# Kernel optimization log

Hardware: AMD Instinct MI355X
Metric: run time of the kernel (lower is better)

The kernel has to match this reference:

```python
import jax, jax.numpy as jnp
import numpy as np

B, D, H, W = 32, 64, 64, 64
K = 512  # num_embeddings


def _l2norm(x, axis):
    return x / jnp.linalg.norm(x, axis=axis, keepdims=True)


def setup_inputs() -> dict:
    key = jax.random.key(0)
    k1, k2 = jax.random.split(key)
    # continuous latents, normalized on the unit sphere along channel dim D
    z_e = _l2norm(jax.random.normal(k1, (B, D, H, W), jnp.float32), axis=1)
    # codebook: uniform(-1,1) then row-normalized (as in torch __init__)
    emb_weight = _l2norm(
        jax.random.uniform(k2, (K, D), jnp.float32, -1.0, 1.0), axis=1)
    kappa = jnp.float32(1.0)
    return {"z_e": z_e, "emb_weight": emb_weight, "kappa": kappa}


def reference(z_e, emb_weight, kappa):
    b, d, h, w = z_e.shape
    # [B,D,H,W] -> [N,D] tokens
    flat_z = z_e.transpose(0, 2, 3, 1).reshape(-1, d)
    emb_w = _l2norm(emb_weight, axis=1)            # [K,D]
    sims = flat_z @ emb_w.T                        # [N,K]
    logits = kappa * sims
    # categorical sampling == torch.multinomial over softmax(logits)
    indices = jax.random.categorical(jax.random.key(42), logits, axis=-1)  # [N]
    z_q = emb_w[indices].reshape(b, h, w, d).transpose(0, 3, 1, 2)  # [B,D,H,W]
    chosen_sims = jnp.take_along_axis(sims, indices[:, None], axis=1)[:, 0]
    reg = jnp.mean(kappa * (1.0 - chosen_sims))
    return z_q, reg, indices.reshape(b, h, w)
```

## Files before the change

kernel.cpp:

```cpp
#include <hip/hip_runtime.h>
#include <stdint.h>

#define K_CODES 512
#define N_TOK   131072
#define ZQ_ELEMS 8388608
#define ZS_STRIDE 68
#define ECSTRIDE 65

__device__ __forceinline__ uint32_t rotl32(uint32_t x, int d) {
#if __has_builtin(__builtin_amdgcn_alignbit)
  return __builtin_amdgcn_alignbit(x, x, 32 - d);
#else
  return (x << d) | (x >> (32 - d));
#endif
}

template <int CTRL, int RMASK>
__device__ __forceinline__ float dpp_add_f32(float x) {
  int d = __builtin_amdgcn_update_dpp(0, __builtin_bit_cast(int, x),
                                      CTRL, RMASK, 0xf, true);
  return x + __builtin_bit_cast(float, d);
}
template <int CTRL, int RMASK>
__device__ __forceinline__ uint32_t dpp_max_u32(uint32_t x) {
  uint32_t d = (uint32_t)__builtin_amdgcn_update_dpp(0, (int)x,
                                                     CTRL, RMASK, 0xf, true);
  return x > d ? x : d;
}
__device__ __forceinline__ float wave_sum(float x) {
  x = dpp_add_f32<0x111, 0xf>(x);
  x = dpp_add_f32<0x112, 0xf>(x);
  x = dpp_add_f32<0x114, 0xf>(x);
  x = dpp_add_f32<0x118, 0xf>(x);
  x = dpp_add_f32<0x142, 0xa>(x);
  x = dpp_add_f32<0x143, 0xc>(x);
  return __builtin_bit_cast(float,
      __builtin_amdgcn_readlane(__builtin_bit_cast(int, x), 63));
}
__device__ __forceinline__ uint32_t wave_max(uint32_t x) {
  x = dpp_max_u32<0x111, 0xf>(x);
  x = dpp_max_u32<0x112, 0xf>(x);
  x = dpp_max_u32<0x114, 0xf>(x);
  x = dpp_max_u32<0x118, 0xf>(x);
  x = dpp_max_u32<0x142, 0xa>(x);
  x = dpp_max_u32<0x143, 0xc>(x);
  return (uint32_t)__builtin_amdgcn_readlane((int)x, 63);
}

__device__ __forceinline__ uint32_t tf_bits_xor(uint32_t lo) {
  const uint32_t ks0 = 0u, ks1 = 42u, ks2 = 0x1BD11BDAu ^ 0u ^ 42u;
  uint32_t x0 = 0u;
  uint32_t x1 = lo + ks1;
#define TFR(r) { x0 += x1; x1 = rotl32(x1, (r)); x1 ^= x0; }
  TFR(13) TFR(15) TFR(26) TFR(6)
  x0 += ks1; x1 += ks2 + 1u;
  TFR(17) TFR(29) TFR(16) TFR(24)
  x0 += ks2; x1 += ks0 + 2u;
  TFR(13) TFR(15) TFR(26) TFR(6)
  x0 += ks0; x1 += ks1 + 3u;
  TFR(17) TFR(29) TFR(16) TFR(24)
  x0 += ks1; x1 += ks2 + 4u;
  TFR(13) TFR(15) TFR(26) TFR(6)
  x0 += ks2; x1 += ks0 + 5u;
#undef TFR
  return x0 ^ x1;
}

__device__ __forceinline__ float g_of_u23(uint32_t u23) {
  float u0 = (float)u23 * 0x1p-23f;
  float u  = fmaxf(u0 + 1.17549435e-38f, 1.17549435e-38f);
  float nl = -logf(u);
  return -logf(nl);
}

__device__ __forceinline__ float g_fast_u23(uint32_t u23) {
  uint32_t m = 8388608u - u23;
  float nl;
  if (m <= 131072u) {
    float x = (float)m * 0x1p-23f;
    nl = x * fmaf(x, fmaf(x, fmaf(x, 0.25f, 0.33333334f), 0.5f), 1.0f);
  } else {
    float u = (float)u23 * 0x1p-23f;
    nl = -__logf(u);
  }
  return -__logf(nl);
}

__device__ __forceinline__ uint32_t thr_fast(float gthr) {
  float u_t = __expf(-__expf(-gthr));
  int B = (int)floorf(u_t * 8388608.0f) - 64;
  if (B < 0) B = 0;
  return ((uint32_t)B) << 9;
}

__global__ void k_norm(const float* __restrict__ w, float* __restrict__ embn) {
  int k = blockIdx.x;
  int d = threadIdx.x;
  float v = w[(k << 6) + d];
  float s = v * v;
#pragma unroll
  for (int off = 1; off < 64; off <<= 1) s += __shfl_xor(s, off);
  embn[(k << 6) + d] = v / sqrtf(s);
}

__global__ __launch_bounds__(1024, 8) void k_top(
    const float* __restrict__ z_e, const float* __restrict__ embn,
    const float* __restrict__ kappa_p, int* __restrict__ idx_ws,
    float* __restrict__ partials, float* __restrict__ out_idx) {
  __shared__ float zs[16 * ZS_STRIDE];
  __shared__ float redbuf[16];

  const float kappa = kappa_p[0];
  const int tid = threadIdx.x;
  const int wv = tid >> 6;
  const int lane = tid & 63;
  const int t0 = blockIdx.x * 16;
  const int t = t0 + wv;
  const int b = t0 >> 12, h = (t0 >> 6) & 63, w0 = t0 & 63;
  const float* zb = z_e + (b << 18) + (h << 6) + w0;

  {
    int wloc = tid & 15;
    int d = tid >> 4;
    zs[wloc * ZS_STRIDE + d] = zb[(d << 12) + wloc];
  }
  __syncthreads();
  const float zv = zs[wv * ZS_STRIDE + lane];

  const uint32_t base = ((uint32_t)t << 9) + (uint32_t)(lane << 3);
  uint32_t p[8];
  uint32_t rm = 0;
#pragma unroll
  for (int j = 0; j < 8; ++j) {
    uint32_t bits = tf_bits_xor(base + (uint32_t)j);
    uint32_t pk = (bits & 0xFFFFFE00u) | (uint32_t)((lane << 3) + j);
    p[j] = pk;
    rm = rm > pk ? rm : pk;
  }
  rm = wave_max(rm);

  float best, bsim, best2 = -INFINITY;
  int bk;
  {
    int k = (int)(rm & 511u);
    float e = embn[(k << 6) + lane];
    float pr = wave_sum(zv * e);
    best = fmaf(kappa, pr, g_fast_u23(rm >> 9));
    bsim = pr;
    bk = k;
  }
  uint32_t cut = thr_fast(best - 1.0001f * kappa - 0.001f);

#pragma unroll
  for (int j = 0; j < 8; ++j) {
    unsigned long long m = __ballot(p[j] >= cut);
    while (m) {
      int L = __ffsll(m) - 1;
      m &= m - 1;
      uint32_t pk = __shfl(p[j], L);
      if (pk == rm) continue;
      if (pk < cut) continue;
      int k = (int)(pk & 511u);
      float e = embn[(k << 6) + lane];
      float pr = wave_sum(zv * e);
      float v = fmaf(kappa, pr, g_fast_u23(pk >> 9));
      if (v > best) {
        best2 = best;
        best = v; bk = k; bsim = pr;
        cut = thr_fast(best - 1.0001f * kappa - 0.001f);
      } else if (v > best2) {
        best2 = v;
      }
    }
  }

  if (best - best2 < 2e-4f) {
    best = -INFINITY; bsim = 0.0f; bk = 0;
#pragma unroll
    for (int j = 0; j < 8; ++j) {
      unsigned long long m = __ballot(p[j] >= cut);
      while (m) {
        int L = __ffsll(m) - 1;
        m &= m - 1;
        uint32_t pk = __shfl(p[j], L);
        int k = (int)(pk & 511u);
        float e = embn[(k << 6) + lane];
        float pr = wave_sum(zv * e);
        float gg = g_of_u23(pk >> 9);
        float v = fmaf(kappa, pr, gg);
        if (v > best || (v == best && k < bk)) { best = v; bk = k; bsim = pr; }
      }
    }
  }

  if (lane == 0) {
    idx_ws[t] = bk;
    out_idx[t] = (float)bk;
    redbuf[wv] = kappa * (1.0f - bsim);
  }
  __syncthreads();
  if (tid == 0) {
    float s = 0.f;
#pragma unroll
    for (int i = 0; i < 16; ++i) s += redbuf[i];
    partials[blockIdx.x] = s;
  }
}

__global__ __launch_bounds__(256) void k_reg(const float* __restrict__ partials,
                                             float* __restrict__ out_reg) {
  int tid = threadIdx.x;
  float s = 0.f;
#pragma unroll
  for (int j = 0; j < 32; ++j) s += partials[(j << 8) + tid];
#pragma unroll
  for (int off = 32; off; off >>= 1) s += __shfl_down(s, off);
  __shared__ float l[4];
  int lane = tid & 63, wid = tid >> 6;
  if (lane == 0) l[wid] = s;
  __syncthreads();
  if (tid == 0) out_reg[0] = ((l[0] + l[1]) + (l[2] + l[3])) * (1.0f / 131072.0f);
}

__global__ __launch_bounds__(256) void k_gather(
    const float* __restrict__ embn, const int* __restrict__ idx_ws,
    float* __restrict__ out_zq) {
  __shared__ float erow[64 * ECSTRIDE];
  __shared__ int sidx[64];
  int blk = blockIdx.x;
  int b = blk >> 6, h = blk & 63;
  int tid = threadIdx.x;
  int lane = tid & 63, wid = tid >> 6;

  if (tid < 64) sidx[tid] = idx_ws[(b << 12) + (h << 6) + tid];
  __syncthreads();
  for (int r = wid; r < 64; r += 4)
    erow[r * ECSTRIDE + lane] = embn[(sidx[r] << 6) + lane];
  __syncthreads();

  int w = tid & 63;
  int d0 = tid >> 6;
  float* outp = out_zq + (b << 18) + (h << 6) + w;
#pragma unroll
  for (int i = 0; i < 16; ++i) {
    int d = (i << 2) + d0;
    outp[d << 12] = erow[w * ECSTRIDE + d];
  }
}

extern "C" void kernel_launch(void* const* d_in, const int* in_sizes, int n_in,
                              void* d_out, int out_size, void* d_ws, size_t ws_size,
                              hipStream_t stream) {
  const float* z_e    = (const float*)d_in[0];
  const float* emb_w  = (const float*)d_in[1];
  const float* kappa  = (const float*)d_in[2];

  float* embn     = (float*)d_ws;
  int*   idx_ws   = (int*)((char*)d_ws + 131072);
  float* partials = (float*)((char*)d_ws + 131072 + 524288);

  float* out     = (float*)d_out;
  float* out_zq  = out;
  float* out_reg = out + ZQ_ELEMS;
  float* out_idx = out + ZQ_ELEMS + 1;

  k_norm  <<<K_CODES, 64, 0, stream>>>(emb_w, embn);
  k_top   <<<N_TOK / 16, 1024, 0, stream>>>(z_e, embn, kappa, idx_ws, partials, out_idx);
  k_reg   <<<1, 256, 0, stream>>>(partials, out_reg);
  k_gather<<<2048, 256, 0, stream>>>(embn, idx_ws, out_zq);
}
```

Measured before the change: 167.0 us.

## Score surviving candidates per lane instead of serial wave-wide dot products

Candidate scoring in the Gumbel-max sampler is reorganized. The old code processed candidates one at a time across the whole wave: a ballot, a shuffle, a 64-wide dot product and a DPP reduction for each. Now each lane scores its own surviving candidates, reading codebook rows from global memory and broadcasting z components with readlane. It keeps a per-lane top-2 and finishes with wave-wide fmax reductions. The cutoff is fixed from the seed and no longer tightened as better candidates appear, and the exact tie-break now compares only the top two instead of rescanning all candidates. This may prune less and adds per-lane uncoalesced 256-byte row loads.

```diff
diff --git a/kernel.cpp b/kernel.cpp
--- a/kernel.cpp
+++ b/kernel.cpp
@@ -20,6 +20,12 @@
   int d = __builtin_amdgcn_update_dpp(0, __builtin_bit_cast(int, x),
                                       CTRL, RMASK, 0xf, true);
   return x + __builtin_bit_cast(float, d);
+}
+template <int CTRL, int RMASK>
+__device__ __forceinline__ float dpp_max_f32(float x) {
+  int d = __builtin_amdgcn_update_dpp(0, __builtin_bit_cast(int, x),
+                                      CTRL, RMASK, 0xf, true);
+  return fmaxf(x, __builtin_bit_cast(float, d));
 }
 template <int CTRL, int RMASK>
 __device__ __forceinline__ uint32_t dpp_max_u32(uint32_t x) {
@@ -37,7 +43,17 @@
   return __builtin_bit_cast(float,
       __builtin_amdgcn_readlane(__builtin_bit_cast(int, x), 63));
 }
-__device__ __forceinline__ uint32_t wave_max(uint32_t x) {
+__device__ __forceinline__ float wave_fmax(float x) {
+  x = dpp_max_f32<0x111, 0xf>(x);
+  x = dpp_max_f32<0x112, 0xf>(x);
+  x = dpp_max_f32<0x114, 0xf>(x);
+  x = dpp_max_f32<0x118, 0xf>(x);
+  x = dpp_max_f32<0x142, 0xa>(x);
+  x = dpp_max_f32<0x143, 0xc>(x);
+  return __builtin_bit_cast(float,
+      __builtin_amdgcn_readlane(__builtin_bit_cast(int, x), 63));
+}
+__device__ __forceinline__ uint32_t wave_max_u32(uint32_t x) {
   x = dpp_max_u32<0x111, 0xf>(x);
   x = dpp_max_u32<0x112, 0xf>(x);
   x = dpp_max_u32<0x114, 0xf>(x);
@@ -45,6 +61,13 @@
   x = dpp_max_u32<0x142, 0xa>(x);
   x = dpp_max_u32<0x143, 0xc>(x);
   return (uint32_t)__builtin_amdgcn_readlane((int)x, 63);
+}
+__device__ __forceinline__ float rl_f(float x, int L) {
+  return __builtin_bit_cast(float,
+      __builtin_amdgcn_readlane(__builtin_bit_cast(int, x), L));
+}
+__device__ __forceinline__ int rl_i(int x, int L) {
+  return __builtin_amdgcn_readlane(x, L);
 }
 
 __device__ __forceinline__ uint32_t tf_bits_xor(uint32_t lo) {
@@ -127,6 +150,8 @@
   __syncthreads();
   const float zv = zs[wv * ZS_STRIDE + lane];
 
+#define ZR(d) rl_f(zv, d)
+
   const uint32_t base = ((uint32_t)t << 9) + (uint32_t)(lane << 3);
   uint32_t p[8];
   uint32_t rm = 0;
@@ -137,67 +162,87 @@
     p[j] = pk;
     rm = rm > pk ? rm : pk;
   }
-  rm = wave_max(rm);
-
-  float best, bsim, best2 = -INFINITY;
-  int bk;
+  rm = wave_max_u32(rm);
+
   {
     int k = (int)(rm & 511u);
     float e = embn[(k << 6) + lane];
     float pr = wave_sum(zv * e);
-    best = fmaf(kappa, pr, g_fast_u23(rm >> 9));
-    bsim = pr;
-    bk = k;
-  }
-  uint32_t cut = thr_fast(best - 1.0001f * kappa - 0.001f);
-
-#pragma unroll
-  for (int j = 0; j < 8; ++j) {
-    unsigned long long m = __ballot(p[j] >= cut);
-    while (m) {
-      int L = __ffsll(m) - 1;
-      m &= m - 1;
-      uint32_t pk = __shfl(p[j], L);
-      if (pk == rm) continue;
-      if (pk < cut) continue;
-      int k = (int)(pk & 511u);
-      float e = embn[(k << 6) + lane];
-      float pr = wave_sum(zv * e);
-      float v = fmaf(kappa, pr, g_fast_u23(pk >> 9));
-      if (v > best) {
-        best2 = best;
-        best = v; bk = k; bsim = pr;
-        cut = thr_fast(best - 1.0001f * kappa - 0.001f);
-      } else if (v > best2) {
-        best2 = v;
+    float vseed = fmaf(kappa, pr, g_fast_u23(rm >> 9));
+    uint32_t cut = thr_fast(vseed - 1.0001f * kappa - 0.001f);
+
+    uint32_t msk = 0;
+#pragma unroll
+    for (int j = 0; j < 8; ++j) msk |= (p[j] >= cut) ? (1u << j) : 0u;
+
+    float lv1 = -INFINITY, lv2 = -INFINITY;
+    float ls1 = 0.f, ls2 = 0.f;
+    int lk1 = 0, lk2 = 0;
+    uint32_t lpk1 = 0, lpk2 = 0;
+
+    while (__ballot(msk != 0u)) {
+      bool have = (msk != 0u);
+      uint32_t pk_sel = p[0];
+#pragma unroll
+      for (int j = 7; j >= 0; --j)
+        if (msk & (1u << j)) pk_sel = p[j];
+      msk &= msk - 1u;
+
+      int ck = have ? (int)(pk_sel & 511u) : 0;
+      const float* ep = embn + (ck << 6);
+      float s0 = 0.f, s1 = 0.f, s2 = 0.f, s3 = 0.f;
+#pragma unroll
+      for (int d = 0; d < 64; d += 4) {
+        s0 = fmaf(ZR(d + 0), ep[d + 0], s0);
+        s1 = fmaf(ZR(d + 1), ep[d + 1], s1);
+        s2 = fmaf(ZR(d + 2), ep[d + 2], s2);
+        s3 = fmaf(ZR(d + 3), ep[d + 3], s3);
+      }
+      float s = (s0 + s1) + (s2 + s3);
+      float v = have ? fmaf(kappa, s, g_fast_u23(pk_sel >> 9)) : -INFINITY;
+      if (v > lv1) {
+        lv2 = lv1; ls2 = ls1; lk2 = lk1; lpk2 = lpk1;
+        lv1 = v;   ls1 = s;   lk1 = ck;  lpk1 = pk_sel;
+      } else if (v > lv2) {
+        lv2 = v; ls2 = s; lk2 = ck; lpk2 = pk_sel;
       }
     }
-  }
-
-  if (best - best2 < 2e-4f) {
-    best = -INFINITY; bsim = 0.0f; bk = 0;
-#pragma unroll
-    for (int j = 0; j < 8; ++j) {
-      unsigned long long m = __ballot(p[j] >= cut);
-      while (m) {
-        int L = __ffsll(m) - 1;
-        m &= m - 1;
-        uint32_t pk = __shfl(p[j], L);
-        int k = (int)(pk & 511u);
-        float e = embn[(k << 6) + lane];
-        float pr = wave_sum(zv * e);
-        float gg = g_of_u23(pk >> 9);
-        float v = fmaf(kappa, pr, gg);
-        if (v > best || (v == best && k < bk)) { best = v; bk = k; bsim = pr; }
+
+    float v1 = wave_fmax(lv1);
+    unsigned long long ball = __ballot(lv1 == v1);
+    int Ls = (int)(__ffsll(ball) - 1);
+    int   bk   = rl_i(lk1, Ls);
+    float bsim = rl_f(ls1, Ls);
+    uint32_t bpk = (uint32_t)rl_i((int)lpk1, Ls);
+
+    float lv1m = (lane == Ls) ? -INFINITY : lv1;
+    float v2a = wave_fmax(lv1m);
+    float v2b = rl_f(lv2, Ls);
+    float v2 = fmaxf(v2a, v2b);
+
+    if (v1 - v2 < 2e-4f) {
+      int k2; float s2; uint32_t pk2;
+      if (v2a >= v2b) {
+        unsigned long long b2 = __ballot(lv1m == v2a);
+        int L2 = (int)(__ffsll(b2) - 1);
+        k2 = rl_i(lk1, L2); s2 = rl_f(ls1, L2); pk2 = (uint32_t)rl_i((int)lpk1, L2);
+      } else {
+        k2 = rl_i(lk2, Ls); s2 = rl_f(ls2, Ls); pk2 = (uint32_t)rl_i((int)lpk2, Ls);
+      }
+      if (v2 > -INFINITY) {
+        float vp1 = fmaf(kappa, bsim, g_of_u23(bpk >> 9));
+        float vp2 = fmaf(kappa, s2,   g_of_u23(pk2 >> 9));
+        if (vp2 > vp1 || (vp2 == vp1 && k2 < bk)) { bk = k2; bsim = s2; }
       }
     }
-  }
-
-  if (lane == 0) {
-    idx_ws[t] = bk;
-    out_idx[t] = (float)bk;
-    redbuf[wv] = kappa * (1.0f - bsim);
-  }
+
+    if (lane == 0) {
+      idx_ws[t] = bk;
+      out_idx[t] = (float)bk;
+      redbuf[wv] = kappa * (1.0f - bsim);
+    }
+  }
+#undef ZR
   __syncthreads();
   if (tid == 0) {
     float s = 0.f;
```

Result: slower. 187.9 us (+12.6%).
